# Optimization experiments

Hardware: AMD Instinct MI355X
Metric: run time of the kernel (lower is better)

Reference implementation:

```python
import jax, jax.numpy as jnp
import numpy as np

N_NODES = 100000
M_COLS = 100000
K = 32
C = 256


def setup_inputs() -> dict:
    key = jax.random.key(0)
    ks = jax.random.split(key, 7)
    return {
        "Wh_neg_real": jax.random.normal(ks[0], (N_NODES, C), dtype=jnp.float32),
        "Wh_neg_imag": jax.random.normal(ks[1], (N_NODES, C), dtype=jnp.float32),
        "N_neg": jax.random.randint(ks[2], (K + 1, M_COLS), 0, N_NODES, dtype=jnp.int64),
        "k_neighbors": K,
        "W_real": jax.random.normal(ks[3], (C, 1), dtype=jnp.float32) * 0.05,
        "W_imag": jax.random.normal(ks[4], (C, 1), dtype=jnp.float32) * 0.05,
        "b_real": jax.random.normal(ks[5], (1,), dtype=jnp.float32) * 0.05,
        "b_imag": jax.random.normal(ks[6], (1,), dtype=jnp.float32) * 0.05,
    }


def reference(Wh_neg_real, Wh_neg_imag, N_neg, k_neighbors, W_real, W_imag, b_real, b_imag):
    # Complex linear (in_channels -> 1): tmp = Wh @ W + b, expanded into real/imag parts.
    tmp_r = Wh_neg_real @ W_real - Wh_neg_imag @ W_imag + b_real  # [N, 1]
    tmp_i = Wh_neg_real @ W_imag + Wh_neg_imag @ W_real + b_imag  # [N, 1]

    center = N_neg[0]                      # [M]
    neigh = N_neg[1:].reshape(-1)          # [k*M]

    Wh1_r = tmp_r[center]                  # [M, 1]
    Wh1_i = tmp_i[center]                  # [M, 1]
    Wh2_r = tmp_r[neigh].reshape(k_neighbors, -1, 1)  # [k, M, 1]
    Wh2_i = tmp_i[neigh].reshape(k_neighbors, -1, 1)  # [k, M, 1]

    # einsum('nc,knc->knc') is a broadcasted elementwise product; squeeze channel (=1).
    attention = jax.nn.relu(Wh1_r[None] * Wh2_r + Wh1_i[None] * Wh2_i)[..., 0]  # [k, M]

    # Normalize each column by its neighbor-sum (+ eps), via reciprocal as in torch.
    return attention * jnp.reciprocal(attention.sum(0) + 0.001)  # [k, M]
```

## Files before the change

kernel.cpp:

```cpp
#include <hip/hip_runtime.h>

#define C_DIM 256
#define K_NEIGH 32

__global__ __launch_bounds__(256) void proj_kernel(
    const float* __restrict__ whr, const float* __restrict__ whi,
    const float* __restrict__ wr,  const float* __restrict__ wi,
    const float* __restrict__ br,  const float* __restrict__ bi,
    float2* __restrict__ tmp, int n_nodes)
{
    const int node = (int)((blockIdx.x * (unsigned)blockDim.x + threadIdx.x) >> 6);
    const int lane = threadIdx.x & 63;
    if (node >= n_nodes) return;

    const float4* whr4 = (const float4*)(whr + (size_t)node * C_DIM);
    const float4* whi4 = (const float4*)(whi + (size_t)node * C_DIM);
    const float4 a = whr4[lane];
    const float4 b = whi4[lane];
    const float4 u = ((const float4*)wr)[lane];
    const float4 v = ((const float4*)wi)[lane];

    float vr = a.x*u.x + a.y*u.y + a.z*u.z + a.w*u.w
             - (b.x*v.x + b.y*v.y + b.z*v.z + b.w*v.w);
    float vi = a.x*v.x + a.y*v.y + a.z*v.z + a.w*v.w
             +  b.x*u.x + b.y*u.y + b.z*u.z + b.w*u.w;

    #pragma unroll
    for (int off = 32; off > 0; off >>= 1) {
        vr += __shfl_xor(vr, off, 64);
        vi += __shfl_xor(vi, off, 64);
    }

    if (lane == 0) {
        tmp[node] = make_float2(vr + br[0], vi + bi[0]);
    }
}

__global__ __launch_bounds__(256) void attn_kernel(
    const int* __restrict__ nneg, const float2* __restrict__ tmp,
    float* __restrict__ out, int m_cols)
{
    const int m = blockIdx.x * blockDim.x + threadIdx.x;
    if (m >= m_cols) return;

    const int cidx = nneg[m];
    const float2 c = tmp[cidx];

    float att[K_NEIGH];
    float s = 0.f;
    #pragma unroll
    for (int k = 0; k < K_NEIGH; ++k) {
        const int idx = nneg[(size_t)(k + 1) * m_cols + m];
        const float2 t = tmp[idx];
        const float a = fmaxf(c.x * t.x + c.y * t.y, 0.f);
        att[k] = a;
        s += a;
    }

    const float r = 1.0f / (s + 0.001f);
    #pragma unroll
    for (int k = 0; k < K_NEIGH; ++k) {
        out[(size_t)k * m_cols + m] = att[k] * r;
    }
}

extern "C" void kernel_launch(void* const* d_in, const int* in_sizes, int n_in,
                              void* d_out, int out_size, void* d_ws, size_t ws_size,
                              hipStream_t stream)
{
    const float* whr = (const float*)d_in[0];
    const float* whi = (const float*)d_in[1];
    const int*   nng = (const int*)d_in[2];
    const float* wr  = (const float*)d_in[4];
    const float* wi  = (const float*)d_in[5];
    const float* br  = (const float*)d_in[6];
    const float* bi  = (const float*)d_in[7];

    const int c_dim   = in_sizes[4];
    const int n_nodes = in_sizes[0] / c_dim;
    const int m_cols  = in_sizes[2] / (K_NEIGH + 1);

    float2* tmp = (float2*)d_ws;

    const int blocksA = (n_nodes + 3) / 4;
    proj_kernel<<<blocksA, 256, 0, stream>>>(whr, whi, wr, wi, br, bi, tmp, n_nodes);

    const int blocksB = (m_cols + 255) / 256;
    attn_kernel<<<blocksB, 256, 0, stream>>>(nng, tmp, (float*)d_out, m_cols);
}
```

Baseline: 52.15 us.

## Split neighbor loop across four wavefronts per column tile with shared-memory sum

The attention kernel now assigns 64 columns per block and splits the 32 neighbors into four groups of eight, one per wavefront. Partial sums are combined through shared memory after a barrier. This launches four times as many blocks and gives more memory-level parallelism for the gathers. Index loads and output stores are also marked nontemporal to avoid polluting cache, at the cost of a block barrier and redundant center loads per wavefront.

Result: slower. 53.67 us (+2.9%).

```diff
diff --git a/kernel.cpp b/kernel.cpp
--- a/kernel.cpp
+++ b/kernel.cpp
@@ -2,6 +2,9 @@
 
 #define C_DIM 256
 #define K_NEIGH 32
+#define KG 4
+#define KPER (K_NEIGH / KG)
+#define COLS_PER_BLOCK 64
 
 __global__ __launch_bounds__(256) void proj_kernel(
     const float* __restrict__ whr, const float* __restrict__ whi,
@@ -13,10 +16,8 @@
     const int lane = threadIdx.x & 63;
     if (node >= n_nodes) return;
 
-    const float4* whr4 = (const float4*)(whr + (size_t)node * C_DIM);
-    const float4* whi4 = (const float4*)(whi + (size_t)node * C_DIM);
-    const float4 a = whr4[lane];
-    const float4 b = whi4[lane];
+    const float4 a = ((const float4*)(whr + (size_t)node * C_DIM))[lane];
+    const float4 b = ((const float4*)(whi + (size_t)node * C_DIM))[lane];
     const float4 u = ((const float4*)wr)[lane];
     const float4 v = ((const float4*)wi)[lane];
 
@@ -40,27 +41,41 @@
     const int* __restrict__ nneg, const float2* __restrict__ tmp,
     float* __restrict__ out, int m_cols)
 {
-    const int m = blockIdx.x * blockDim.x + threadIdx.x;
-    if (m >= m_cols) return;
+    const int ml = threadIdx.x & 63;
+    const int kg = threadIdx.x >> 6;
+    const int m  = blockIdx.x * COLS_PER_BLOCK + ml;
 
-    const int cidx = nneg[m];
-    const float2 c = tmp[cidx];
+    __shared__ float part[KG][COLS_PER_BLOCK];
 
-    float att[K_NEIGH];
+    float att[KPER];
     float s = 0.f;
-    #pragma unroll
-    for (int k = 0; k < K_NEIGH; ++k) {
-        const int idx = nneg[(size_t)(k + 1) * m_cols + m];
-        const float2 t = tmp[idx];
-        const float a = fmaxf(c.x * t.x + c.y * t.y, 0.f);
-        att[k] = a;
-        s += a;
+    float2 c = make_float2(0.f, 0.f);
+
+    if (m < m_cols) {
+        const int cidx = __builtin_nontemporal_load(&nneg[m]);
+        c = tmp[cidx];
+
+        #pragma unroll
+        for (int j = 0; j < KPER; ++j) {
+            const int row = 1 + kg * KPER + j;
+            const int idx = __builtin_nontemporal_load(&nneg[(size_t)row * m_cols + m]);
+            const float2 t = tmp[idx];
+            const float a = fmaxf(c.x * t.x + c.y * t.y, 0.f);
+            att[j] = a;
+            s += a;
+        }
     }
+    part[kg][ml] = s;
+    __syncthreads();
 
-    const float r = 1.0f / (s + 0.001f);
-    #pragma unroll
-    for (int k = 0; k < K_NEIGH; ++k) {
-        out[(size_t)k * m_cols + m] = att[k] * r;
+    if (m < m_cols) {
+        const float stot = part[0][ml] + part[1][ml] + part[2][ml] + part[3][ml];
+        const float r = 1.0f / (stot + 0.001f);
+        #pragma unroll
+        for (int j = 0; j < KPER; ++j) {
+            const int k = kg * KPER + j;
+            __builtin_nontemporal_store(att[j] * r, &out[(size_t)k * m_cols + m]);
+        }
     }
 }
 
@@ -85,6 +100,6 @@
     const int blocksA = (n_nodes + 3) / 4;
     proj_kernel<<<blocksA, 256, 0, stream>>>(whr, whi, wr, wi, br, bi, tmp, n_nodes);
 
-    const int blocksB = (m_cols + 255) / 256;
+    const int blocksB = (m_cols + COLS_PER_BLOCK - 1) / COLS_PER_BLOCK;
     attn_kernel<<<blocksB, 256, 0, stream>>>(nng, tmp, (float*)d_out, m_cols);
 }
```

## Fuse projection and attention into persistent kernel with grid barrier

Applied to the files above, without the earlier changes.

Merges the two kernels into one persistent kernel of 1024 blocks. Blocks first run a grid-stride projection loop with a software-prefetched next row, then prefetch their neighbor indices with nontemporal loads before a global atomic barrier. After the barrier they gather and normalize, using nontemporal stores for the output. The aim is to hide the index loads behind the barrier wait and drop one launch. In exchange it needs all blocks co-resident to avoid deadlock and adds a memset launch plus barrier spin cost.

After: 155.6 us. +198.4%, slower.

```diff
diff --git a/kernel.cpp b/kernel.cpp
--- a/kernel.cpp
+++ b/kernel.cpp
@@ -2,65 +2,120 @@
 
 #define C_DIM 256
 #define K_NEIGH 32
+#define GRID_BLKS 1024
+#define BLK_THR 256
 
-__global__ __launch_bounds__(256) void proj_kernel(
+__global__ __launch_bounds__(BLK_THR, 4) void fused_kernel(
     const float* __restrict__ whr, const float* __restrict__ whi,
+    const int*   __restrict__ nneg,
     const float* __restrict__ wr,  const float* __restrict__ wi,
     const float* __restrict__ br,  const float* __restrict__ bi,
-    float2* __restrict__ tmp, int n_nodes)
+    float2* __restrict__ tmp, unsigned int* __restrict__ bar,
+    float* __restrict__ out, int n_nodes, int m_cols)
 {
-    const int node = (int)((blockIdx.x * (unsigned)blockDim.x + threadIdx.x) >> 6);
-    const int lane = threadIdx.x & 63;
-    if (node >= n_nodes) return;
+    const int gtid   = blockIdx.x * BLK_THR + threadIdx.x;
+    const int gsz    = GRID_BLKS * BLK_THR;
+    const int lane   = threadIdx.x & 63;
+    const int wave   = gtid >> 6;
+    const int nwaves = gsz >> 6;
 
-    const float4* whr4 = (const float4*)(whr + (size_t)node * C_DIM);
-    const float4* whi4 = (const float4*)(whi + (size_t)node * C_DIM);
-    const float4 a = whr4[lane];
-    const float4 b = whi4[lane];
-    const float4 u = ((const float4*)wr)[lane];
-    const float4 v = ((const float4*)wi)[lane];
+    {
+        const float4 u  = ((const float4*)wr)[lane];
+        const float4 v  = ((const float4*)wi)[lane];
+        const float br0 = br[0];
+        const float bi0 = bi[0];
 
-    float vr = a.x*u.x + a.y*u.y + a.z*u.z + a.w*u.w
-             - (b.x*v.x + b.y*v.y + b.z*v.z + b.w*v.w);
-    float vi = a.x*v.x + a.y*v.y + a.z*v.z + a.w*v.w
-             +  b.x*u.x + b.y*u.y + b.z*u.z + b.w*u.w;
+        int node = wave;
+        float4 a, b;
+        if (node < n_nodes) {
+            a = ((const float4*)(whr + (size_t)node * C_DIM))[lane];
+            b = ((const float4*)(whi + (size_t)node * C_DIM))[lane];
+        }
+        while (node < n_nodes) {
+            const int nnode = node + nwaves;
+            float4 an, bn;
+            if (nnode < n_nodes) {
+                an = ((const float4*)(whr + (size_t)nnode * C_DIM))[lane];
+                bn = ((const float4*)(whi + (size_t)nnode * C_DIM))[lane];
+            }
 
-    #pragma unroll
-    for (int off = 32; off > 0; off >>= 1) {
-        vr += __shfl_xor(vr, off, 64);
-        vi += __shfl_xor(vi, off, 64);
+            float vr = a.x*u.x + a.y*u.y + a.z*u.z + a.w*u.w
+                     - (b.x*v.x + b.y*v.y + b.z*v.z + b.w*v.w);
+            float vi = a.x*v.x + a.y*v.y + a.z*v.z + a.w*v.w
+                     +  b.x*u.x + b.y*u.y + b.z*u.z + b.w*u.w;
+
+            #pragma unroll
+            for (int off = 32; off > 0; off >>= 1) {
+                vr += __shfl_xor(vr, off, 64);
+                vi += __shfl_xor(vi, off, 64);
+            }
+            if (lane == 0) {
+                tmp[node] = make_float2(vr + br0, vi + bi0);
+            }
+
+            node = nnode;
+            a = an;
+            b = bn;
+        }
     }
 
-    if (lane == 0) {
-        tmp[node] = make_float2(vr + br[0], vi + bi[0]);
-    }
-}
-
-__global__ __launch_bounds__(256) void attn_kernel(
-    const int* __restrict__ nneg, const float2* __restrict__ tmp,
-    float* __restrict__ out, int m_cols)
-{
-    const int m = blockIdx.x * blockDim.x + threadIdx.x;
-    if (m >= m_cols) return;
-
-    const int cidx = nneg[m];
-    const float2 c = tmp[cidx];
-
-    float att[K_NEIGH];
-    float s = 0.f;
-    #pragma unroll
-    for (int k = 0; k < K_NEIGH; ++k) {
-        const int idx = nneg[(size_t)(k + 1) * m_cols + m];
-        const float2 t = tmp[idx];
-        const float a = fmaxf(c.x * t.x + c.y * t.y, 0.f);
-        att[k] = a;
-        s += a;
+    const int m = gtid;
+    int cidx = 0;
+    int idx[K_NEIGH];
+    if (m < m_cols) {
+        cidx = __builtin_nontemporal_load(&nneg[m]);
+        #pragma unroll
+        for (int k = 0; k < K_NEIGH; ++k) {
+            idx[k] = __builtin_nontemporal_load(&nneg[(size_t)(k + 1) * m_cols + m]);
+        }
     }
 
-    const float r = 1.0f / (s + 0.001f);
-    #pragma unroll
-    for (int k = 0; k < K_NEIGH; ++k) {
-        out[(size_t)k * m_cols + m] = att[k] * r;
+    __syncthreads();
+    if (threadIdx.x == 0) {
+        __builtin_amdgcn_fence(__ATOMIC_RELEASE, "agent");
+        __hip_atomic_fetch_add(bar, 1u, __ATOMIC_RELAXED, __HIP_MEMORY_SCOPE_AGENT);
+        while (__hip_atomic_load(bar, __ATOMIC_RELAXED, __HIP_MEMORY_SCOPE_AGENT)
+               < (unsigned)GRID_BLKS) {
+            __builtin_amdgcn_s_sleep(2);
+        }
+        __builtin_amdgcn_fence(__ATOMIC_ACQUIRE, "agent");
+    }
+    __syncthreads();
+
+    if (m < m_cols) {
+        const float2 c = tmp[cidx];
+        float att[K_NEIGH];
+        float s = 0.f;
+        #pragma unroll
+        for (int k = 0; k < K_NEIGH; ++k) {
+            const float2 t = tmp[idx[k]];
+            const float a = fmaxf(c.x * t.x + c.y * t.y, 0.f);
+            att[k] = a;
+            s += a;
+        }
+        const float r = 1.0f / (s + 0.001f);
+        #pragma unroll
+        for (int k = 0; k < K_NEIGH; ++k) {
+            __builtin_nontemporal_store(att[k] * r, &out[(size_t)k * m_cols + m]);
+        }
+    }
+
+    for (int m2 = gtid + gsz; m2 < m_cols; m2 += gsz) {
+        const float2 c = tmp[nneg[m2]];
+        float att[K_NEIGH];
+        float s = 0.f;
+        #pragma unroll
+        for (int k = 0; k < K_NEIGH; ++k) {
+            const float2 t = tmp[nneg[(size_t)(k + 1) * m_cols + m2]];
+            const float a = fmaxf(c.x * t.x + c.y * t.y, 0.f);
+            att[k] = a;
+            s += a;
+        }
+        const float r = 1.0f / (s + 0.001f);
+        #pragma unroll
+        for (int k = 0; k < K_NEIGH; ++k) {
+            __builtin_nontemporal_store(att[k] * r, &out[(size_t)k * m_cols + m2]);
+        }
     }
 }
 
@@ -76,15 +131,16 @@
     const float* br  = (const float*)d_in[6];
     const float* bi  = (const float*)d_in[7];
 
-    const int c_dim   = in_sizes[4];
-    const int n_nodes = in_sizes[0] / c_dim;
+    const int n_nodes = in_sizes[0] / in_sizes[4];
     const int m_cols  = in_sizes[2] / (K_NEIGH + 1);
 
     float2* tmp = (float2*)d_ws;
+    const size_t coff = ((size_t)n_nodes * sizeof(float2) + 255) & ~(size_t)255;
+    unsigned int* bar = (unsigned int*)((char*)d_ws + coff);
 
-    const int blocksA = (n_nodes + 3) / 4;
-    proj_kernel<<<blocksA, 256, 0, stream>>>(whr, whi, wr, wi, br, bi, tmp, n_nodes);
+    hipMemsetAsync(bar, 0, 256, stream);
 
-    const int blocksB = (m_cols + 255) / 256;
-    attn_kernel<<<blocksB, 256, 0, stream>>>(nng, tmp, (float*)d_out, m_cols);
+    fused_kernel<<<GRID_BLKS, BLK_THR, 0, stream>>>(
+        whr, whi, nng, wr, wi, br, bi, tmp, bar, (float*)d_out,
+        n_nodes, m_cols);
 }
```
